# Kernel optimization log

Hardware: AMD Instinct MI355X
Metric: run time of the kernel (lower is better)

## Reference

```python
import jax, jax.numpy as jnp
import numpy as np

NEG_INF = -jnp.inf


def _rope(x, cos, sin):
    # x: (B, S, H, D); cos/sin: (1, S, 1, D//2)
    xr = x.reshape(*x.shape[:-1], -1, 2)
    x1, x2 = xr[..., 0], xr[..., 1]  # (B, S, H, D//2) each
    # faithful to source: concat halves along last axis, same total size D
    return jnp.concatenate([x1 * cos - x2 * sin, x1 * sin + x2 * cos], axis=-1)


def setup_inputs() -> dict:
    B, S, D, H, Ld = 2, 2048, 2048, 16, 128
    key = jax.random.key(0)
    ks = jax.random.split(key, 6)
    sc = 1.0 / np.sqrt(D)
    return {
        "x": jax.random.normal(ks[0], (B, S, D), jnp.float32),
        "attn_mask": jnp.ones((B, S), jnp.int32),
        "Wq": jax.random.normal(ks[1], (D, H * Ld), jnp.float32) * sc,
        "bq": jnp.zeros((H * Ld,), jnp.float32),
        "Wk": jax.random.normal(ks[2], (D, H * Ld), jnp.float32) * sc,
        "bk": jnp.zeros((H * Ld,), jnp.float32),
        "Wv": jax.random.normal(ks[3], (D, H * Ld), jnp.float32) * sc,
        "bv": jnp.zeros((H * Ld,), jnp.float32),
        "Wo": jax.random.normal(ks[4], (H * Ld, D), jnp.float32) * sc,
        "bo": jnp.zeros((D,), jnp.float32),
        "num_heads": H,
    }


def reference(x, attn_mask, Wq, bq, Wk, bk, Wv, bv, Wo, bo, num_heads):
    B, S, D = x.shape
    H = int(num_heads)
    Ld = Wq.shape[1] // H
    base = 10000

    q = (x @ Wq + bq).reshape(B, S, H, Ld)
    k = (x @ Wk + bk).reshape(B, S, H, Ld)
    v = (x @ Wv + bv).reshape(B, S, H, Ld)

    # rotary tables (match RotaryEmbedding.setup, sliced to seq_len)
    inv_freq = 1.0 / base ** (2 * jnp.arange(0, Ld // 2) / Ld)
    angles = jnp.arange(S)[:, None] * inv_freq[None, :]  # (S, Ld//2)
    cos = jnp.cos(angles)[None, :, None, :].astype(x.dtype)
    sin = jnp.sin(angles)[None, :, None, :].astype(x.dtype)
    q = _rope(q, cos, sin)
    k = _rope(k, cos, sin)

    q = jnp.transpose(q, (0, 2, 1, 3))  # (B, H, S, Ld)
    k = jnp.transpose(k, (0, 2, 1, 3))
    v = jnp.transpose(v, (0, 2, 1, 3))

    scale = jnp.sqrt(jnp.float32(Ld)).astype(x.dtype)
    scores = jnp.einsum('bnqd,bnkd->bnqk', q, k) / scale  # (B, H, S, S)

    # faithful mask from source: keep where arange[None,:] >= arange[:,None]
    row_idx = jnp.arange(S)[None, :]
    col_idx = jnp.arange(S)[:, None]
    keep = row_idx >= col_idx  # (S, S)
    scores = jnp.where(keep[None, None, :, :], scores, NEG_INF)

    # padding mask applied over the QUERY axis, as in source: (B,1,S,1)
    scores = jnp.where(attn_mask[:, None, :, None] > 0, scores, NEG_INF)

    attn = jax.nn.softmax(scores, axis=-1)
    attended = jnp.einsum('bnqk,bnkd->bnqd', attn, v)
    attended = jnp.transpose(attended, (0, 2, 1, 3)).reshape(B, S, H * Ld)
    return attended @ Wo + bo
```

## Files before the change

kernel.cpp:

```cpp
#include <hip/hip_runtime.h>
#include <math.h>

typedef __bf16 bf16x8 __attribute__((ext_vector_type(8)));
typedef float f32x4 __attribute__((ext_vector_type(4)));

#define MFMA_BF16(a,b,c) __builtin_amdgcn_mfma_f32_16x16x32_bf16((a),(b),(c),0,0,0)

static constexpr int S_LEN = 2048;
static constexpr int DM    = 2048;
static constexpr int NHEAD = 16;
static constexpr int LDH   = 128;
static constexpr int BATCH = 2;
static constexpr size_t QKV_SEG = (size_t)BATCH * NHEAD * S_LEN * LDH;

__device__ __forceinline__ unsigned short f2bf(float f) {
    unsigned u = __float_as_uint(f);
    u += 0x7fffu + ((u >> 16) & 1u);
    return (unsigned short)(u >> 16);
}
__device__ __forceinline__ float bf2f(unsigned short h) {
    return __uint_as_float(((unsigned)h) << 16);
}
__device__ __forceinline__ float fexp2(float x) { return exp2f(x); }

__device__ __forceinline__ void ld_lds16(const void* g, void* l) {
    __builtin_amdgcn_global_load_lds(
        (const __attribute__((address_space(1))) unsigned int*)g,
        (__attribute__((address_space(3))) unsigned int*)l, 16, 0, 0);
}

__global__ void prep_all(const float* __restrict__ x, unsigned short* __restrict__ xb,
                         float* __restrict__ ct, float* __restrict__ st,
                         const float* __restrict__ W0, const float* __restrict__ W1,
                         const float* __restrict__ W2, const float* __restrict__ W3,
                         unsigned short* __restrict__ O0, unsigned short* __restrict__ O1,
                         unsigned short* __restrict__ O2, unsigned short* __restrict__ O3) {
    __shared__ unsigned short tile[32][33];
    int bid = blockIdx.x;
    int t = threadIdx.x;
    if (bid < 8192) {
        int idx = bid * 256 + t;
        float4 v = reinterpret_cast<const float4*>(x)[idx];
        unsigned lo = (unsigned)f2bf(v.x) | ((unsigned)f2bf(v.y) << 16);
        unsigned hi = (unsigned)f2bf(v.z) | ((unsigned)f2bf(v.w) << 16);
        reinterpret_cast<uint2*>(xb)[idx] = make_uint2(lo, hi);
    } else if (bid < 8704) {
        int i = t & 63;
        int s = (bid - 8192) * 4 + (t >> 6);
        float freq = (float)exp(-(double)(2 * i) / 128.0 * 9.210340371976184);
        float a = (float)s * freq;
        ct[s * 64 + i] = cosf(a);
        st[s * 64 + i] = sinf(a);
    } else {
        int wid = bid - 8704;
        int z = wid >> 12;
        int rem = wid & 4095;
        int k0 = (rem >> 6) * 32;
        int n0 = (rem & 63) * 32;
        const float* W = (z == 0) ? W0 : (z == 1) ? W1 : (z == 2) ? W2 : W3;
        unsigned short* Wt = (z == 0) ? O0 : (z == 1) ? O1 : (z == 2) ? O2 : O3;
        int ir = t >> 3, ic = (t & 7) * 4;
        float4 v = *reinterpret_cast<const float4*>(&W[(size_t)(k0 + ir) * DM + n0 + ic]);
        tile[ir][ic + 0] = f2bf(v.x);
        tile[ir][ic + 1] = f2bf(v.y);
        tile[ir][ic + 2] = f2bf(v.z);
        tile[ir][ic + 3] = f2bf(v.w);
        __syncthreads();
        unsigned lo = (unsigned)tile[ic + 0][ir] | ((unsigned)tile[ic + 1][ir] << 16);
        unsigned hi = (unsigned)tile[ic + 2][ir] | ((unsigned)tile[ic + 3][ir] << 16);
        *reinterpret_cast<uint2*>(&Wt[(size_t)(n0 + ir) * DM + k0 + ic]) = make_uint2(lo, hi);
    }
}

__global__ __launch_bounds__(256, 2) void gemm_out_v2(
    const unsigned short* __restrict__ A,
    const unsigned short* __restrict__ Bt,
    const float* __restrict__ b0,
    float* __restrict__ outp)
{
    constexpr int K  = DM;
    constexpr int NT = K / 32;
    constexpr int SLOT_B = 24576;
    __shared__ __attribute__((aligned(16))) unsigned short smem[36864];

    int t = threadIdx.x, lane = t & 63, w = t >> 6;
    int i16 = lane & 15, quad = lane >> 4;
    int wc = w & 1, wr = w >> 1;

    int flat = blockIdx.y * 16 + blockIdx.x;
    int xcd = flat & 7, r8 = flat >> 3;
    int nbx = xcd * 2 + (r8 >> 4);
    int nby = r8 & 15;
    int m0 = nby * 256, n0 = nbx * 128;

    const unsigned short* ga[4];
    const unsigned short* gb[2];
    int loffA[4], loffB[2];
#pragma unroll
    for (int j = 0; j < 4; ++j) {
        int off = j * 4096 + t * 16;
        int row = off >> 6;
        int g = ((off >> 4) & 3) ^ ((row >> 1) & 3);
        ga[j] = A + (size_t)(m0 + row) * K + g * 8;
        loffA[j] = off;
    }
#pragma unroll
    for (int j = 0; j < 2; ++j) {
        int off = j * 4096 + t * 16;
        int row = off >> 6;
        int g = ((off >> 4) & 3) ^ ((row >> 1) & 3);
        gb[j] = Bt + (size_t)(n0 + row) * K + g * 8;
        loffB[j] = off;
    }

    auto stage = [&](int slot, int kt) {
        char* base = (char*)smem + slot * SLOT_B;
#pragma unroll
        for (int j = 0; j < 4; ++j)
            ld_lds16(ga[j] + kt * 32, base + loffA[j]);
#pragma unroll
        for (int j = 0; j < 2; ++j)
            ld_lds16(gb[j] + kt * 32, base + 16384 + loffB[j]);
    };

    f32x4 acc[8][4];
    const f32x4 z4 = {0.f, 0.f, 0.f, 0.f};
#pragma unroll
    for (int mi = 0; mi < 8; ++mi)
#pragma unroll
        for (int ni = 0; ni < 4; ++ni) acc[mi][ni] = z4;

    auto compute = [&](int slot) {
        const char* Ab = (const char*)smem + slot * SLOT_B;
        const char* Bb = Ab + 16384;
        bf16x8 bF[4];
#pragma unroll
        for (int ni = 0; ni < 4; ++ni) {
            int rB = wc * 64 + ni * 16 + i16;
            bF[ni] = *reinterpret_cast<const bf16x8*>(
                Bb + rB * 64 + ((quad ^ ((rB >> 1) & 3)) * 16));
        }
#pragma unroll
        for (int h = 0; h < 2; ++h) {
            bf16x8 aF[4];
#pragma unroll
            for (int mi = 0; mi < 4; ++mi) {
                int rA = wr * 128 + h * 64 + mi * 16 + i16;
                aF[mi] = *reinterpret_cast<const bf16x8*>(
                    Ab + rA * 64 + ((quad ^ ((rA >> 1) & 3)) * 16));
            }
            __builtin_amdgcn_s_setprio(1);
#pragma unroll
            for (int mi = 0; mi < 4; ++mi)
#pragma unroll
                for (int ni = 0; ni < 4; ++ni)
                    acc[h * 4 + mi][ni] = MFMA_BF16(aF[mi], bF[ni], acc[h * 4 + mi][ni]);
            __builtin_amdgcn_s_setprio(0);
        }
    };

    stage(0, 0); stage(1, 1);
    asm volatile("s_waitcnt vmcnt(6)" ::: "memory");
    __builtin_amdgcn_s_barrier();
    asm volatile("" ::: "memory");

    int cs = 0, ssl = 2;
    for (int tt = 0; tt < NT - 2; ++tt) {
        stage(ssl, tt + 2);
        compute(cs);
        asm volatile("s_waitcnt vmcnt(6)" ::: "memory");
        __builtin_amdgcn_s_barrier();
        asm volatile("" ::: "memory");
        cs  = (cs  == 2) ? 0 : cs  + 1;
        ssl = (ssl == 2) ? 0 : ssl + 1;
    }
    compute(cs);
    asm volatile("s_waitcnt vmcnt(0)" ::: "memory");
    __builtin_amdgcn_s_barrier();
    asm volatile("" ::: "memory");
    cs = (cs == 2) ? 0 : cs + 1;
    compute(cs);

#pragma unroll
    for (int mi = 0; mi < 8; ++mi)
#pragma unroll
        for (int ni = 0; ni < 4; ++ni) {
            int nn = n0 + wc * 64 + ni * 16 + i16;
            float bv = b0[nn];
#pragma unroll
            for (int r = 0; r < 4; ++r) {
                int mm = m0 + wr * 128 + mi * 16 + quad * 4 + r;
                outp[(size_t)mm * DM + nn] = acc[mi][ni][r] + bv;
            }
        }
}

__global__ __launch_bounds__(256, 2) void gemm_qkv_v2(
    const unsigned short* __restrict__ A,
    const unsigned short* __restrict__ Bt,
    const float* __restrict__ b0, const float* __restrict__ b1,
    const float* __restrict__ b2,
    const float* __restrict__ ctab, const float* __restrict__ stab,
    unsigned short* __restrict__ outp)
{
    constexpr int K  = DM;
    constexpr int NT = K / 32;
    constexpr int SLOT_B = 24576;
    __shared__ __attribute__((aligned(16))) unsigned short smem[36864];

    int t = threadIdx.x, lane = t & 63, w = t >> 6;
    int i16 = lane & 15, quad = lane >> 4;
    int wc = w & 1, wr = w >> 1;

    int flat = blockIdx.y * 48 + blockIdx.x;
    int xcd = flat & 7, r8 = flat >> 3;
    int nbx = xcd * 6 + (r8 >> 4);
    int nby = r8 & 15;
    int m0 = nby * 256, n0 = nbx * 128;

    const unsigned short* ga[4];
    const unsigned short* gb[2];
    int loffA[4], loffB[2];
#pragma unroll
    for (int j = 0; j < 4; ++j) {
        int off = j * 4096 + t * 16;
        int row = off >> 6;
        int g = ((off >> 4) & 3) ^ ((row >> 1) & 3);
        ga[j] = A + (size_t)(m0 + row) * K + g * 8;
        loffA[j] = off;
    }
#pragma unroll
    for (int j = 0; j < 2; ++j) {
        int off = j * 4096 + t * 16;
        int row = off >> 6;
        int g = ((off >> 4) & 3) ^ ((row >> 1) & 3);
        gb[j] = Bt + (size_t)(n0 + row) * K + g * 8;
        loffB[j] = off;
    }

    auto stage = [&](int slot, int kt) {
        char* base = (char*)smem + slot * SLOT_B;
#pragma unroll
        for (int j = 0; j < 4; ++j)
            ld_lds16(ga[j] + kt * 32, base + loffA[j]);
#pragma unroll
        for (int j = 0; j < 2; ++j)
            ld_lds16(gb[j] + kt * 32, base + 16384 + loffB[j]);
    };

    f32x4 acc[8][4];
    const f32x4 z4 = {0.f, 0.f, 0.f, 0.f};
#pragma unroll
    for (int mi = 0; mi < 8; ++mi)
#pragma unroll
        for (int ni = 0; ni < 4; ++ni) acc[mi][ni] = z4;

    auto compute = [&](int slot) {
        const char* Ab = (const char*)smem + slot * SLOT_B;
        const char* Bb = Ab + 16384;
        bf16x8 bF[4];
#pragma unroll
        for (int ni = 0; ni < 4; ++ni) {
            int rB = wc * 64 + ni * 16 + i16;
            bF[ni] = *reinterpret_cast<const bf16x8*>(
                Bb + rB * 64 + ((quad ^ ((rB >> 1) & 3)) * 16));
        }
#pragma unroll
        for (int h = 0; h < 2; ++h) {
            bf16x8 aF[4];
#pragma unroll
            for (int mi = 0; mi < 4; ++mi) {
                int rA = wr * 128 + h * 64 + mi * 16 + i16;
                aF[mi] = *reinterpret_cast<const bf16x8*>(
                    Ab + rA * 64 + ((quad ^ ((rA >> 1) & 3)) * 16));
            }
            __builtin_amdgcn_s_setprio(1);
#pragma unroll
            for (int mi = 0; mi < 4; ++mi)
#pragma unroll
                for (int ni = 0; ni < 4; ++ni)
                    acc[h * 4 + mi][ni] = MFMA_BF16(aF[mi], bF[ni], acc[h * 4 + mi][ni]);
            __builtin_amdgcn_s_setprio(0);
        }
    };

    stage(0, 0); stage(1, 1);
    asm volatile("s_waitcnt vmcnt(6)" ::: "memory");
    __builtin_amdgcn_s_barrier();
    asm volatile("" ::: "memory");

    int cs = 0, ssl = 2;
    for (int tt = 0; tt < NT - 2; ++tt) {
        stage(ssl, tt + 2);
        compute(cs);
        asm volatile("s_waitcnt vmcnt(6)" ::: "memory");
        __builtin_amdgcn_s_barrier();
        asm volatile("" ::: "memory");
        cs  = (cs  == 2) ? 0 : cs  + 1;
        ssl = (ssl == 2) ? 0 : ssl + 1;
    }
    compute(cs);
    asm volatile("s_waitcnt vmcnt(0)" ::: "memory");
    __builtin_amdgcn_s_barrier();
    asm volatile("" ::: "memory");
    cs = (cs == 2) ? 0 : cs + 1;
    compute(cs);
    __syncthreads();

    unsigned short* Cs = smem;
    int which = n0 >> 11;
    int hh = (n0 & 2047) >> 7;
    const float* bp = (which == 0) ? b0 : ((which == 1) ? b1 : b2);
    int segn = n0 & 2047;
    int bb = m0 >> 11, s0 = m0 & 2047;

    if (which == 2) {
#pragma unroll
        for (int mi = 0; mi < 8; ++mi)
#pragma unroll
            for (int ni = 0; ni < 4; ++ni) {
                int d = wc * 64 + ni * 16 + i16;
                float bv = bp[segn + d];
#pragma unroll
                for (int r = 0; r < 4; ++r) {
                    int sl = wr * 128 + mi * 16 + quad * 4 + r;
                    Cs[d * 256 + (((sl >> 3) ^ (d & 31)) * 8) + (sl & 7)] =
                        f2bf(acc[mi][ni][r] + bv);
                }
            }
        __syncthreads();
        unsigned short* vout = outp + 2 * QKV_SEG;
#pragma unroll
        for (int it = 0; it < 16; ++it) {
            int idx = it * 256 + t;
            int d = idx >> 5, sg = idx & 31;
            uint4 v = *reinterpret_cast<const uint4*>(
                &Cs[d * 256 + ((sg ^ (d & 31)) * 8)]);
            size_t oidx = (((size_t)(bb * NHEAD + hh)) * LDH + d) * S_LEN + s0 + sg * 8;
            *reinterpret_cast<uint4*>(vout + oidx) = v;
        }
    } else {
#pragma unroll
        for (int mi = 0; mi < 8; ++mi)
#pragma unroll
            for (int ni = 0; ni < 4; ++ni) {
                int nl = wc * 64 + ni * 16 + i16;
                float bv = bp[segn + nl];
#pragma unroll
                for (int r = 0; r < 4; ++r) {
                    int ml = wr * 128 + mi * 16 + quad * 4 + r;
                    Cs[ml * 128 + nl] = f2bf(acc[mi][ni][r] + bv);
                }
            }
        __syncthreads();
        float qscale = (which == 0) ? (0.08838834764831845f * 1.4426950408889634f) : 1.0f;
        unsigned short* qout = outp + (size_t)which * QKV_SEG;
#pragma unroll
        for (int it = 0; it < 16; ++it) {
            int idx = it * 256 + t;
            int row = idx >> 4, c16 = idx & 15;
            int mm = m0 + row;
            int ss = mm & 2047, bb2 = mm >> 11;
            int i8 = (c16 & 7) * 8;
            const unsigned short* crow = Cs + row * 128 + i8 * 2;
            uint4 w0 = *reinterpret_cast<const uint4*>(crow);
            uint4 w1 = *reinterpret_cast<const uint4*>(crow + 8);
            unsigned pw[8] = {w0.x, w0.y, w0.z, w0.w, w1.x, w1.y, w1.z, w1.w};
            float4 cA = *reinterpret_cast<const float4*>(&ctab[ss * 64 + i8]);
            float4 cB = *reinterpret_cast<const float4*>(&ctab[ss * 64 + i8 + 4]);
            float4 sA = *reinterpret_cast<const float4*>(&stab[ss * 64 + i8]);
            float4 sB = *reinterpret_cast<const float4*>(&stab[ss * 64 + i8 + 4]);
            float cv[8] = {cA.x, cA.y, cA.z, cA.w, cB.x, cB.y, cB.z, cB.w};
            float sv[8] = {sA.x, sA.y, sA.z, sA.w, sB.x, sB.y, sB.z, sB.w};
            bool hi = (c16 >= 8);
            unsigned short ov[8];
#pragma unroll
            for (int j = 0; j < 8; ++j) {
                float xe = bf2f((unsigned short)(pw[j] & 0xffff));
                float xo = bf2f((unsigned short)(pw[j] >> 16));
                float o = hi ? (xe * sv[j] + xo * cv[j]) : (xe * cv[j] - xo * sv[j]);
                ov[j] = f2bf(o * qscale);
            }
            size_t oidx = (((size_t)(bb2 * NHEAD + hh)) * S_LEN + ss) * LDH + c16 * 8;
            *reinterpret_cast<uint4*>(qout + oidx) =
                *reinterpret_cast<const uint4*>(ov);
        }
    }
}

__global__ __launch_bounds__(256, 2) void attn_kernel(
    const unsigned short* __restrict__ q,
    const unsigned short* __restrict__ k,
    const unsigned short* __restrict__ vt,
    unsigned short* __restrict__ att)
{
    __shared__ __attribute__((aligned(16))) unsigned short Ks[2][64 * 128];
    __shared__ __attribute__((aligned(16))) unsigned short Vs[2][128 * 64];
    __shared__ __attribute__((aligned(16))) unsigned short Ps[4][32 * 64];

    int bid = blockIdx.x;
    int second = bid >> 8;
    int p = bid & 255;
    int xb = second ? (15 - (p >> 5)) : (p >> 5);
    int bh = p & 31;
    int b = bh >> 4, h = bh & (NHEAD - 1);
    int q0 = xb * 128;

    int t = threadIdx.x, w = t >> 6, lane = t & 63;
    int i16 = lane & 15, quad = lane >> 4;
    int qbase = q0 + w * 32;

    bf16x8 qf[2][4];
#pragma unroll
    for (int qs = 0; qs < 2; ++qs) {
        const unsigned short* qrow = q + ((size_t)bh * S_LEN + qbase + qs * 16 + i16) * LDH;
#pragma unroll
        for (int c = 0; c < 4; ++c)
            qf[qs][c] = *reinterpret_cast<const bf16x8*>(qrow + c * 32 + quad * 8);
    }

    const f32x4 z4 = {0.f, 0.f, 0.f, 0.f};
    f32x4 o[2][8];
#pragma unroll
    for (int qs = 0; qs < 2; ++qs)
#pragma unroll
        for (int dt = 0; dt < 8; ++dt) o[qs][dt] = z4;
    float l_i[2] = {0.f, 0.f};

    const unsigned short* kbh  = k  + (size_t)bh * S_LEN * LDH;
    const unsigned short* vtbh = vt + (size_t)bh * LDH * S_LEN;
    unsigned short* PsW = Ps[w];

    auto stage = [&](int buf, int kk0) {
#pragma unroll
        for (int j = 0; j < 4; ++j) {
            int off = j * 4096 + w * 1024 + lane * 16;
            int key = off >> 8;
            int gk = ((off >> 4) & 15) ^ (key & 15);
            ld_lds16(&kbh[(size_t)(kk0 + key) * LDH + gk * 8], (char*)Ks[buf] + off);
            int d = off >> 7;
            int gv = ((off >> 4) & 7) ^ (d & 7);
            ld_lds16(&vtbh[(size_t)d * S_LEN + kk0 + gv * 8], (char*)Vs[buf] + off);
        }
    };

    stage(0, q0);
    int nch = (S_LEN - q0) >> 6;
    for (int ci = 0; ci < nch; ++ci) {
        __syncthreads();
        if (ci + 1 < nch) stage((ci + 1) & 1, q0 + (ci + 1) * 64);
        int kk0 = q0 + ci * 64;
        if (kk0 + 64 <= qbase) continue;
        const unsigned short* Kb = Ks[ci & 1];
        const unsigned short* Vb = Vs[ci & 1];

        f32x4 s[2][4];
#pragma unroll
        for (int qs = 0; qs < 2; ++qs)
#pragma unroll
            for (int kn = 0; kn < 4; ++kn) s[qs][kn] = z4;
#pragma unroll
        for (int c = 0; c < 4; ++c) {
            bf16x8 kf[4];
#pragma unroll
            for (int kn = 0; kn < 4; ++kn) {
                int key = kn * 16 + i16;
                int gs = (c * 4 + quad) ^ (key & 15);
                kf[kn] = *reinterpret_cast<const bf16x8*>((const char*)Kb + key * 256 + gs * 16);
            }
            __builtin_amdgcn_s_setprio(1);
#pragma unroll
            for (int qs = 0; qs < 2; ++qs)
#pragma unroll
                for (int kn = 0; kn < 4; ++kn)
                    s[qs][kn] = MFMA_BF16(kf[kn], qf[qs][c], s[qs][kn]);
            __builtin_amdgcn_s_setprio(0);
        }

        bool diag = (kk0 < qbase + 32);
#pragma unroll
        for (int qs = 0; qs < 2; ++qs) {
            int q_local = qs * 16 + i16;
            int qg = qbase + q_local;
#pragma unroll
            for (int kn = 0; kn < 4; ++kn) {
                int keyb = kk0 + kn * 16 + quad * 4;
                float pv[4];
                if (diag) {
#pragma unroll
                    for (int r = 0; r < 4; ++r)
                        pv[r] = (keyb + r >= qg) ? fexp2(s[qs][kn][r]) : 0.f;
                } else {
#pragma unroll
                    for (int r = 0; r < 4; ++r) pv[r] = fexp2(s[qs][kn][r]);
                }
                l_i[qs] += (pv[0] + pv[1]) + (pv[2] + pv[3]);
                unsigned lo = (unsigned)f2bf(pv[0]) | ((unsigned)f2bf(pv[1]) << 16);
                unsigned hi = (unsigned)f2bf(pv[2]) | ((unsigned)f2bf(pv[3]) << 16);
                int g = (kn * 2 + (quad >> 1)) ^ (q_local & 7);
                char* addr = (char*)PsW + q_local * 128 + g * 16 + (quad & 1) * 8;
                *reinterpret_cast<uint2*>(addr) = make_uint2(lo, hi);
            }
        }

#pragma unroll
        for (int hh = 0; hh < 2; ++hh) {
            bf16x8 pf[2];
#pragma unroll
            for (int qs = 0; qs < 2; ++qs) {
                int q_local = qs * 16 + i16;
                int g = (hh * 4 + quad) ^ (q_local & 7);
                pf[qs] = *reinterpret_cast<const bf16x8*>((const char*)PsW + q_local * 128 + g * 16);
            }
            __builtin_amdgcn_s_setprio(1);
#pragma unroll
            for (int dt = 0; dt < 8; ++dt) {
                int d = dt * 16 + i16;
                int gv = (hh * 4 + quad) ^ (d & 7);
                bf16x8 vf = *reinterpret_cast<const bf16x8*>((const char*)Vb + d * 128 + gv * 16);
                o[0][dt] = MFMA_BF16(pf[0], vf, o[0][dt]);
                o[1][dt] = MFMA_BF16(pf[1], vf, o[1][dt]);
            }
            __builtin_amdgcn_s_setprio(0);
        }
    }

#pragma unroll
    for (int qs = 0; qs < 2; ++qs) {
        float lr = l_i[qs];
        lr += __shfl_xor(lr, 16);
        lr += __shfl_xor(lr, 32);
        l_i[qs] = lr;
    }
#pragma unroll
    for (int qs = 0; qs < 2; ++qs) {
#pragma unroll
        for (int r = 0; r < 4; ++r) {
            float lv = __shfl(l_i[qs], quad * 4 + r);
            float inv = 1.0f / lv;
            int qrow = qbase + qs * 16 + quad * 4 + r;
            unsigned short* orow = att + ((size_t)b * S_LEN + qrow) * DM + h * LDH;
#pragma unroll
            for (int dt = 0; dt < 8; ++dt)
                orow[dt * 16 + i16] = f2bf(o[qs][dt][r] * inv);
        }
    }
}

extern "C" void kernel_launch(void* const* d_in, const int* in_sizes, int n_in,
                              void* d_out, int out_size, void* d_ws, size_t ws_size,
                              hipStream_t stream) {
    const float* x  = (const float*)d_in[0];
    const float* Wq = (const float*)d_in[2];
    const float* bq = (const float*)d_in[3];
    const float* Wk = (const float*)d_in[4];
    const float* bk = (const float*)d_in[5];
    const float* Wv = (const float*)d_in[6];
    const float* bv = (const float*)d_in[7];
    const float* Wo = (const float*)d_in[8];
    const float* bo = (const float*)d_in[9];

    char* ws = (char*)d_ws;
    unsigned short* xb  = (unsigned short*)(ws);
    unsigned short* Wqt = (unsigned short*)(ws + 16777216);
    unsigned short* Wkt = (unsigned short*)(ws + 25165824);
    unsigned short* Wvt = (unsigned short*)(ws + 33554432);
    unsigned short* Wot = (unsigned short*)(ws + 41943040);
    unsigned short* qkv = (unsigned short*)(ws + 50331648);
    unsigned short* att = (unsigned short*)(ws + 100663296);
    float* ctab = (float*)(ws + 117440512);
    float* stab = (float*)(ws + 117964800);

    prep_all<<<25088, 256, 0, stream>>>(x, xb, ctab, stab,
                                        Wq, Wk, Wv, Wo, Wqt, Wkt, Wvt, Wot);

    gemm_qkv_v2<<<dim3(48, 16), 256, 0, stream>>>(
        xb, Wqt, bq, bk, bv, ctab, stab, qkv);

    attn_kernel<<<512, 256, 0, stream>>>(qkv, qkv + QKV_SEG, qkv + 2 * QKV_SEG, att);

    gemm_out_v2<<<dim3(16, 16), 256, 0, stream>>>(att, Wot, bo, (float*)d_out);
}
```

Baseline: 383.1 us.

## Interleave global-to-LDS loads with MFMA halves in QKV GEMM main loop

The QKV GEMM main loop now inlines the stage and compute steps, splitting each K-tile into two halves. Each half issues its LDS fragment reads, then part of the next tile's global-to-LDS loads, then a barrier-guarded MFMA burst at raised priority. The aim is to overlap memory traffic with matrix work more finely, in a ping-pong style across the waves of a block. It adds extra barriers per iteration, which could add sync overhead.

```diff
diff --git a/kernel.cpp b/kernel.cpp
--- a/kernel.cpp
+++ b/kernel.cpp
@@ -195,7 +195,7 @@
         }
 }
 
-__global__ __launch_bounds__(256, 2) void gemm_qkv_v2(
+__global__ __launch_bounds__(256, 2) void gemm_qkv_v4(
     const unsigned short* __restrict__ A,
     const unsigned short* __restrict__ Bt,
     const float* __restrict__ b0, const float* __restrict__ b1,
@@ -291,11 +291,62 @@
 
     int cs = 0, ssl = 2;
     for (int tt = 0; tt < NT - 2; ++tt) {
-        stage(ssl, tt + 2);
-        compute(cs);
+        const char* Ab = (const char*)smem + cs * SLOT_B;
+        const char* Bb = Ab + 16384;
+        char* sbase = (char*)smem + ssl * SLOT_B;
+
+        bf16x8 bF[4], aF[4];
+#pragma unroll
+        for (int ni = 0; ni < 4; ++ni) {
+            int rB = wc * 64 + ni * 16 + i16;
+            bF[ni] = *reinterpret_cast<const bf16x8*>(
+                Bb + rB * 64 + ((quad ^ ((rB >> 1) & 3)) * 16));
+        }
+#pragma unroll
+        for (int mi = 0; mi < 4; ++mi) {
+            int rA = wr * 128 + mi * 16 + i16;
+            aF[mi] = *reinterpret_cast<const bf16x8*>(
+                Ab + rA * 64 + ((quad ^ ((rA >> 1) & 3)) * 16));
+        }
+        ld_lds16(ga[0] + (tt + 2) * 32, sbase + loffA[0]);
+        ld_lds16(ga[1] + (tt + 2) * 32, sbase + loffA[1]);
+        ld_lds16(gb[0] + (tt + 2) * 32, sbase + 16384 + loffB[0]);
+        __builtin_amdgcn_s_barrier();
+        asm volatile("s_waitcnt lgkmcnt(0)" ::: "memory");
+        __builtin_amdgcn_sched_barrier(0);
+        __builtin_amdgcn_s_setprio(1);
+#pragma unroll
+        for (int mi = 0; mi < 4; ++mi)
+#pragma unroll
+            for (int ni = 0; ni < 4; ++ni)
+                acc[mi][ni] = MFMA_BF16(aF[mi], bF[ni], acc[mi][ni]);
+        __builtin_amdgcn_s_setprio(0);
+        __builtin_amdgcn_s_barrier();
+        asm volatile("" ::: "memory");
+
+#pragma unroll
+        for (int mi = 0; mi < 4; ++mi) {
+            int rA = wr * 128 + 64 + mi * 16 + i16;
+            aF[mi] = *reinterpret_cast<const bf16x8*>(
+                Ab + rA * 64 + ((quad ^ ((rA >> 1) & 3)) * 16));
+        }
+        ld_lds16(ga[2] + (tt + 2) * 32, sbase + loffA[2]);
+        ld_lds16(ga[3] + (tt + 2) * 32, sbase + loffA[3]);
+        ld_lds16(gb[1] + (tt + 2) * 32, sbase + 16384 + loffB[1]);
         asm volatile("s_waitcnt vmcnt(6)" ::: "memory");
         __builtin_amdgcn_s_barrier();
+        asm volatile("s_waitcnt lgkmcnt(0)" ::: "memory");
+        __builtin_amdgcn_sched_barrier(0);
+        __builtin_amdgcn_s_setprio(1);
+#pragma unroll
+        for (int mi = 0; mi < 4; ++mi)
+#pragma unroll
+            for (int ni = 0; ni < 4; ++ni)
+                acc[4 + mi][ni] = MFMA_BF16(aF[mi], bF[ni], acc[4 + mi][ni]);
+        __builtin_amdgcn_s_setprio(0);
+        __builtin_amdgcn_s_barrier();
         asm volatile("" ::: "memory");
+
         cs  = (cs  == 2) ? 0 : cs  + 1;
         ssl = (ssl == 2) ? 0 : ssl + 1;
     }
@@ -574,7 +625,7 @@
     prep_all<<<25088, 256, 0, stream>>>(x, xb, ctab, stab,
                                         Wq, Wk, Wv, Wo, Wqt, Wkt, Wvt, Wot);
 
-    gemm_qkv_v2<<<dim3(48, 16), 256, 0, stream>>>(
+    gemm_qkv_v4<<<dim3(48, 16), 256, 0, stream>>>(
         xb, Wqt, bq, bk, bv, ctab, stab, qkv);
 
     attn_kernel<<<512, 256, 0, stream>>>(qkv, qkv + QKV_SEG, qkv + 2 * QKV_SEG, att);
```

After: 385.9 us. About the same (+0.7%).
